# Optimization experiments

Measured on AMD Instinct MI355X. Metric: run time of the kernel, lower is better.

Reference implementation:

```python
import jax, jax.numpy as jnp
import numpy as np

NFFT = 512
SHIFT = 160
EPS = 1e-07
LOG10 = float(np.log(10.0))


def setup_inputs() -> dict:
    key = jax.random.key(0)
    x = jax.random.normal(key, (32, 1, 96512), dtype=jnp.float32)
    n = np.arange(NFFT)
    ang = 2.0 * np.pi * np.outer(n, n) / NFFT  # [k, n]
    W_real = np.cos(ang).astype(np.float32)
    W_imag = (-np.sin(ang)).astype(np.float32)
    return {"x": x, "W_real": jnp.asarray(W_real), "W_imag": jnp.asarray(W_imag)}


def reference(x, W_real, W_imag):
    # x: [B, C, T]; W_real/W_imag: [nfft, nfft] DFT basis (kernel k over taps n)
    B, C, T = x.shape
    n_frames = (T - NFFT) // SHIFT + 1
    # strided frame extraction == Conv1d(stride=SHIFT, kernel=NFFT) unfolding
    idx = jnp.arange(n_frames)[:, None] * SHIFT + jnp.arange(NFFT)[None, :]  # [F, N]
    frames = x[:, :, idx]  # [B, C, F, N]
    real = jnp.einsum('bcfn,kn->bckf', frames, W_real)  # [B, C, nfft, F]
    imag = jnp.einsum('bcfn,kn->bckf', frames, W_imag)
    # mode == 'log': log10 of magnitude spectrogram (with epsilon inside sqrt)
    fft = jnp.log(jnp.sqrt(real * real + imag * imag + EPS)) / LOG10
    fft = fft[:, :, : NFFT // 2, :]  # keep lower half of spectrum
    # normalize_feature: zero-mean, unit-std over frequency axis (biased std)
    mean = jnp.mean(fft, axis=2, keepdims=True)
    std = jnp.std(fft, axis=2, keepdims=True)
    return (fft - mean) / (std + EPS)
```

## Files before the change

kernel.cpp:

```cpp
#include <hip/hip_runtime.h>
#include <stdint.h>

#define TLEN    96512
#define NBATCH  32
#define KOUT    256
#define SHIFT   160
#define NFRAMES 601
#define FT      61
#define NTILES  10
#define NKS     16
#define EPSF    1e-7f

typedef _Float16 f16;
typedef _Float16 half8 __attribute__((ext_vector_type(8)));
typedef float f32x16 __attribute__((ext_vector_type(16)));

#define SPAN      ((FT - 1) * SHIFT + 256)
#define UNITS     (SPAN / 8)
#define PLANE_B   (UNITS * 16)
#define LDS_RED   (4 * PLANE_B)
#define LDS_STAT  (LDS_RED + 2048)
#define LDS_TOTAL (LDS_STAT + 512)

__global__ __launch_bounds__(256) void split_w_kernel(
    const float* __restrict__ Wr, const float* __restrict__ Wi,
    f16* __restrict__ wsW)
{
    int id   = blockIdx.x * 256 + threadIdx.x;
    int lane = id & 63;
    int hl   = (id >> 6) & 1;
    int ri   = (id >> 7) & 1;
    int ks   = (id >> 8) & 15;
    int J    = (id >> 12) & 3;
    int par  = (id >> 14) & 1;
    int l31  = lane & 31, lhi = lane >> 5;
    int k = 2 * (J * 32 + l31) + par;
    int n = ks * 16 + lhi * 8;
    const float* src = (ri ? Wi : Wr) + k * 512 + n;
    f16 v[8];
    #pragma unroll
    for (int j = 0; j < 8; ++j) {
        float xv = src[j];
        f16 h = (f16)xv;
        v[j] = hl ? (f16)(xv - (float)h) : h;
    }
    int c = ((par * 4 + J) * 16 + ks) * 4 + ri * 2 + hl;
    *(half8*)(wsW + (size_t)c * 512 + (l31 * 2 + lhi) * 8) = *(half8*)v;
}

__device__ __forceinline__ void load_a(half8 (&a)[2][2][2],
    const f16* __restrict__ wsW, int par, int jb2, int laneoff, int ks)
{
    #pragma unroll
    for (int m = 0; m < 2; ++m)
      #pragma unroll
      for (int ri = 0; ri < 2; ++ri)
        #pragma unroll
        for (int hl = 0; hl < 2; ++hl) {
            int c = ((par * 4 + jb2 + m) * 16 + ks) * 4 + ri * 2 + hl;
            a[m][ri][hl] = *(const half8*)(wsW + (size_t)c * 512 + laneoff);
        }
}

__device__ __forceinline__ void load_b(half8 (&bb)[2][2],
    const char* smem, int par, int l31, int lhi, int ks)
{
    #pragma unroll
    for (int nf = 0; nf < 2; ++nf)
      #pragma unroll
      for (int hl = 0; hl < 2; ++hl) {
          int u  = (nf * 32 + l31) * 20 + ks * 2 + lhi;
          int up = u ^ ((u >> 3) & 7);
          bb[nf][hl] = *(const half8*)(smem + (par * 2 + hl) * PLANE_B + up * 16);
      }
}

__device__ __forceinline__ void do_mfma(f32x16 (&acc)[2][2][2],
    const half8 (&a)[2][2][2], const half8 (&bb)[2][2])
{
    #pragma unroll
    for (int m = 0; m < 2; ++m)
      #pragma unroll
      for (int nf = 0; nf < 2; ++nf)
        #pragma unroll
        for (int ri = 0; ri < 2; ++ri) {
            acc[m][nf][ri] = __builtin_amdgcn_mfma_f32_32x32x16_f16(
                a[m][ri][0], bb[nf][0], acc[m][nf][ri], 0, 0, 0);
            acc[m][nf][ri] = __builtin_amdgcn_mfma_f32_32x32x16_f16(
                a[m][ri][0], bb[nf][1], acc[m][nf][ri], 0, 0, 0);
            acc[m][nf][ri] = __builtin_amdgcn_mfma_f32_32x32x16_f16(
                a[m][ri][1], bb[nf][0], acc[m][nf][ri], 0, 0, 0);
        }
}

__global__ __launch_bounds__(256, 2) void dft_mfma_kernel(
    const f16* __restrict__ wsW, const float* __restrict__ x,
    float* __restrict__ out)
{
    __shared__ uint4 smem4[LDS_TOTAL / 16];
    char* smem = (char*)smem4;

    const int tid  = threadIdx.x;
    const int lane = tid & 63;
    const int w    = tid >> 6;
    const int l31  = lane & 31;
    const int lhi  = lane >> 5;
    const int b    = blockIdx.y;
    const int f0   = blockIdx.x * FT;
    const int par  = w & 1;
    const int jb2  = (w >> 1) * 2;
    const int laneoff = (l31 * 2 + lhi) * 8;

    half8 a0[2][2][2], a1[2][2][2], b0[2][2], b1[2][2];
    load_a(a0, wsW, par, jb2, laneoff, 0);

    {
        const float* __restrict__ xb = x + (size_t)b * TLEN;
        const int t0 = f0 * SHIFT;
        for (int u = tid; u < UNITS; u += 256) {
            int t = t0 + u * 8;
            float va[8], vb[8];
            if (t + 264 <= TLEN) {
                float4 p0 = *(const float4*)(xb + t);
                float4 p1 = *(const float4*)(xb + t + 4);
                float4 q0 = *(const float4*)(xb + t + 256);
                float4 q1 = *(const float4*)(xb + t + 260);
                va[0]=p0.x; va[1]=p0.y; va[2]=p0.z; va[3]=p0.w;
                va[4]=p1.x; va[5]=p1.y; va[6]=p1.z; va[7]=p1.w;
                vb[0]=q0.x; vb[1]=q0.y; vb[2]=q0.z; vb[3]=q0.w;
                vb[4]=q1.x; vb[5]=q1.y; vb[6]=q1.z; vb[7]=q1.w;
            } else {
                #pragma unroll
                for (int j = 0; j < 8; ++j) {
                    int ta = t + j, tb = t + 256 + j;
                    va[j] = (ta < TLEN) ? xb[ta] : 0.f;
                    vb[j] = (tb < TLEN) ? xb[tb] : 0.f;
                }
            }
            f16 eh[8], el[8], oh[8], ol[8];
            #pragma unroll
            for (int j = 0; j < 8; ++j) {
                float E = va[j] + vb[j], O = va[j] - vb[j];
                eh[j] = (f16)E; el[j] = (f16)(E - (float)eh[j]);
                oh[j] = (f16)O; ol[j] = (f16)(O - (float)oh[j]);
            }
            int up = u ^ ((u >> 3) & 7);
            *(half8*)(smem + 0 * PLANE_B + up * 16) = *(half8*)eh;
            *(half8*)(smem + 1 * PLANE_B + up * 16) = *(half8*)el;
            *(half8*)(smem + 2 * PLANE_B + up * 16) = *(half8*)oh;
            *(half8*)(smem + 3 * PLANE_B + up * 16) = *(half8*)ol;
        }
    }
    __syncthreads();

    f32x16 acc[2][2][2] = {};
    load_b(b0, smem, par, l31, lhi, 0);

    #pragma unroll
    for (int ks2 = 0; ks2 < NKS; ks2 += 2) {
        load_a(a1, wsW, par, jb2, laneoff, ks2 + 1);
        load_b(b1, smem, par, l31, lhi, ks2 + 1);
        do_mfma(acc, a0, b0);
        int k2 = (ks2 + 2 < NKS) ? ks2 + 2 : NKS - 1;
        load_a(a0, wsW, par, jb2, laneoff, k2);
        load_b(b0, smem, par, l31, lhi, k2);
        do_mfma(acc, a1, b1);
    }

    const float C = 0.15051499783199057f;
    float lg[2][2][16];
    float s1[2] = {0.f, 0.f}, s2[2] = {0.f, 0.f};
    #pragma unroll
    for (int m = 0; m < 2; ++m)
      #pragma unroll
      for (int nf = 0; nf < 2; ++nf)
        #pragma unroll
        for (int r = 0; r < 16; ++r) {
            float re = acc[m][nf][0][r], im = acc[m][nf][1][r];
            float lv = C * __log2f(re * re + im * im + EPSF);
            lg[m][nf][r] = lv;
            s1[nf] += lv;
            s2[nf] += lv * lv;
        }
    #pragma unroll
    for (int nf = 0; nf < 2; ++nf) {
        s1[nf] += __shfl_xor(s1[nf], 32);
        s2[nf] += __shfl_xor(s2[nf], 32);
    }
    float2* red = (float2*)(smem + LDS_RED);
    if (lane < 32) {
        red[(w * 2 + 0) * 32 + l31] = make_float2(s1[0], s2[0]);
        red[(w * 2 + 1) * 32 + l31] = make_float2(s1[1], s2[1]);
    }
    __syncthreads();
    float* stat = (float*)(smem + LDS_STAT);
    if (tid < 64) {
        float S1 = 0.f, S2 = 0.f;
        int nf = tid >> 5, c = tid & 31;
        #pragma unroll
        for (int ww = 0; ww < 4; ++ww) {
            float2 p = red[(ww * 2 + nf) * 32 + c];
            S1 += p.x; S2 += p.y;
        }
        float mean = S1 * (1.f / 256.f);
        float var  = fmaxf(S2 * (1.f / 256.f) - mean * mean, 0.f);
        stat[tid]      = mean;
        stat[64 + tid] = 1.f / (__builtin_sqrtf(var) + EPSF);
    }
    __syncthreads();

    #pragma unroll
    for (int nf = 0; nf < 2; ++nf) {
        int fl = nf * 32 + l31;
        int f  = f0 + fl;
        if (fl >= FT || f >= NFRAMES) continue;
        float mean = stat[fl], rstd = stat[64 + fl];
        #pragma unroll
        for (int m = 0; m < 2; ++m)
          #pragma unroll
          for (int r = 0; r < 16; ++r) {
              int k = 2 * ((w >> 1) * 64 + m * 32 + (r & 3) + 8 * (r >> 2) + 4 * lhi) + par;
              out[((size_t)b * KOUT + k) * NFRAMES + f] = (lg[m][nf][r] - mean) * rstd;
          }
    }
}

extern "C" void kernel_launch(void* const* d_in, const int* in_sizes, int n_in,
                              void* d_out, int out_size, void* d_ws, size_t ws_size,
                              hipStream_t stream) {
    const float* x  = (const float*)d_in[0];
    const float* Wr = (const float*)d_in[1];
    const float* Wi = (const float*)d_in[2];
    float* out = (float*)d_out;

    f16* wsW = (f16*)d_ws;

    split_w_kernel<<<128, 256, 0, stream>>>(Wr, Wi, wsW);

    dim3 grid(NTILES, NBATCH);
    dft_mfma_kernel<<<grid, 256, 0, stream>>>(wsW, x, out);
}
```

Baseline: 37.40 us.

## Retile DFT kernel to 76-frame tiles with 512-thread blocks filling one wave

Changes the frame tiling from 10 tiles of 61 frames to 8 tiles of 76 frames and doubles the block to 512 threads. Each wave now owns one 32-row k-block and three 32-frame N fragments instead of two k-blocks and two N fragments. The goal is a grid of 256 blocks, one per CU, so no CUs sit partly idle as they do with the uneven 320-block grid. In exchange, frames 76–95 of each tile are computed and thrown away, and their B operands read past the end of each LDS plane into the next one. The LDS footprint also grows to roughly 110 KB per block, and each wave reuses its A operands less.

```diff
diff --git a/kernel.cpp b/kernel.cpp
--- a/kernel.cpp
+++ b/kernel.cpp
@@ -6,8 +6,8 @@
 #define KOUT    256
 #define SHIFT   160
 #define NFRAMES 601
-#define FT      61
-#define NTILES  10
+#define FT      76
+#define NTILES  8
 #define NKS     16
 #define EPSF    1e-7f
 
@@ -15,12 +15,12 @@
 typedef _Float16 half8 __attribute__((ext_vector_type(8)));
 typedef float f32x16 __attribute__((ext_vector_type(16)));
 
-#define SPAN      ((FT - 1) * SHIFT + 256)
-#define UNITS     (SPAN / 8)
-#define PLANE_B   (UNITS * 16)
-#define LDS_RED   (4 * PLANE_B)
-#define LDS_STAT  (LDS_RED + 2048)
-#define LDS_TOTAL (LDS_STAT + 512)
+#define SPAN       ((FT - 1) * SHIFT + 256)
+#define UNITS      (SPAN / 8)
+#define PLANE_B    24576
+#define LDS_RED    104768
+#define LDS_STAT   (LDS_RED + 6144)
+#define LDS_TOTAL  (LDS_STAT + 768)
 
 __global__ __launch_bounds__(256) void split_w_kernel(
     const float* __restrict__ Wr, const float* __restrict__ Wi,
@@ -48,25 +48,23 @@
     *(half8*)(wsW + (size_t)c * 512 + (l31 * 2 + lhi) * 8) = *(half8*)v;
 }
 
-__device__ __forceinline__ void load_a(half8 (&a)[2][2][2],
-    const f16* __restrict__ wsW, int par, int jb2, int laneoff, int ks)
-{
-    #pragma unroll
-    for (int m = 0; m < 2; ++m)
-      #pragma unroll
-      for (int ri = 0; ri < 2; ++ri)
-        #pragma unroll
-        for (int hl = 0; hl < 2; ++hl) {
-            int c = ((par * 4 + jb2 + m) * 16 + ks) * 4 + ri * 2 + hl;
-            a[m][ri][hl] = *(const half8*)(wsW + (size_t)c * 512 + laneoff);
-        }
-}
-
-__device__ __forceinline__ void load_b(half8 (&bb)[2][2],
+__device__ __forceinline__ void load_a(half8 (&a)[2][2],
+    const f16* __restrict__ wsW, int par, int J, int laneoff, int ks)
+{
+    #pragma unroll
+    for (int ri = 0; ri < 2; ++ri)
+      #pragma unroll
+      for (int hl = 0; hl < 2; ++hl) {
+          int c = ((par * 4 + J) * 16 + ks) * 4 + ri * 2 + hl;
+          a[ri][hl] = *(const half8*)(wsW + (size_t)c * 512 + laneoff);
+      }
+}
+
+__device__ __forceinline__ void load_b(half8 (&bb)[3][2],
     const char* smem, int par, int l31, int lhi, int ks)
 {
     #pragma unroll
-    for (int nf = 0; nf < 2; ++nf)
+    for (int nf = 0; nf < 3; ++nf)
       #pragma unroll
       for (int hl = 0; hl < 2; ++hl) {
           int u  = (nf * 32 + l31) * 20 + ks * 2 + lhi;
@@ -75,25 +73,23 @@
       }
 }
 
-__device__ __forceinline__ void do_mfma(f32x16 (&acc)[2][2][2],
-    const half8 (&a)[2][2][2], const half8 (&bb)[2][2])
-{
-    #pragma unroll
-    for (int m = 0; m < 2; ++m)
-      #pragma unroll
-      for (int nf = 0; nf < 2; ++nf)
-        #pragma unroll
-        for (int ri = 0; ri < 2; ++ri) {
-            acc[m][nf][ri] = __builtin_amdgcn_mfma_f32_32x32x16_f16(
-                a[m][ri][0], bb[nf][0], acc[m][nf][ri], 0, 0, 0);
-            acc[m][nf][ri] = __builtin_amdgcn_mfma_f32_32x32x16_f16(
-                a[m][ri][0], bb[nf][1], acc[m][nf][ri], 0, 0, 0);
-            acc[m][nf][ri] = __builtin_amdgcn_mfma_f32_32x32x16_f16(
-                a[m][ri][1], bb[nf][0], acc[m][nf][ri], 0, 0, 0);
-        }
-}
-
-__global__ __launch_bounds__(256, 2) void dft_mfma_kernel(
+__device__ __forceinline__ void do_mfma(f32x16 (&acc)[3][2],
+    const half8 (&a)[2][2], const half8 (&bb)[3][2])
+{
+    #pragma unroll
+    for (int nf = 0; nf < 3; ++nf)
+      #pragma unroll
+      for (int ri = 0; ri < 2; ++ri) {
+          acc[nf][ri] = __builtin_amdgcn_mfma_f32_32x32x16_f16(
+              a[ri][0], bb[nf][0], acc[nf][ri], 0, 0, 0);
+          acc[nf][ri] = __builtin_amdgcn_mfma_f32_32x32x16_f16(
+              a[ri][0], bb[nf][1], acc[nf][ri], 0, 0, 0);
+          acc[nf][ri] = __builtin_amdgcn_mfma_f32_32x32x16_f16(
+              a[ri][1], bb[nf][0], acc[nf][ri], 0, 0, 0);
+      }
+}
+
+__global__ __launch_bounds__(512, 2) void dft_mfma_kernel(
     const f16* __restrict__ wsW, const float* __restrict__ x,
     float* __restrict__ out)
 {
@@ -108,16 +104,16 @@
     const int b    = blockIdx.y;
     const int f0   = blockIdx.x * FT;
     const int par  = w & 1;
-    const int jb2  = (w >> 1) * 2;
+    const int J    = w >> 1;
     const int laneoff = (l31 * 2 + lhi) * 8;
 
-    half8 a0[2][2][2], a1[2][2][2], b0[2][2], b1[2][2];
-    load_a(a0, wsW, par, jb2, laneoff, 0);
+    half8 a0[2][2], a1[2][2], b0[3][2], b1[3][2];
+    load_a(a0, wsW, par, J, laneoff, 0);
 
     {
         const float* __restrict__ xb = x + (size_t)b * TLEN;
         const int t0 = f0 * SHIFT;
-        for (int u = tid; u < UNITS; u += 256) {
+        for (int u = tid; u < UNITS; u += 512) {
             int t = t0 + u * 8;
             float va[8], vb[8];
             if (t + 264 <= TLEN) {
@@ -153,75 +149,72 @@
     }
     __syncthreads();
 
-    f32x16 acc[2][2][2] = {};
+    f32x16 acc[3][2] = {};
     load_b(b0, smem, par, l31, lhi, 0);
 
     #pragma unroll
     for (int ks2 = 0; ks2 < NKS; ks2 += 2) {
-        load_a(a1, wsW, par, jb2, laneoff, ks2 + 1);
+        load_a(a1, wsW, par, J, laneoff, ks2 + 1);
         load_b(b1, smem, par, l31, lhi, ks2 + 1);
         do_mfma(acc, a0, b0);
         int k2 = (ks2 + 2 < NKS) ? ks2 + 2 : NKS - 1;
-        load_a(a0, wsW, par, jb2, laneoff, k2);
+        load_a(a0, wsW, par, J, laneoff, k2);
         load_b(b0, smem, par, l31, lhi, k2);
         do_mfma(acc, a1, b1);
     }
 
     const float C = 0.15051499783199057f;
-    float lg[2][2][16];
-    float s1[2] = {0.f, 0.f}, s2[2] = {0.f, 0.f};
-    #pragma unroll
-    for (int m = 0; m < 2; ++m)
-      #pragma unroll
-      for (int nf = 0; nf < 2; ++nf)
-        #pragma unroll
-        for (int r = 0; r < 16; ++r) {
-            float re = acc[m][nf][0][r], im = acc[m][nf][1][r];
-            float lv = C * __log2f(re * re + im * im + EPSF);
-            lg[m][nf][r] = lv;
-            s1[nf] += lv;
-            s2[nf] += lv * lv;
-        }
-    #pragma unroll
-    for (int nf = 0; nf < 2; ++nf) {
+    float lg[3][16];
+    float s1[3] = {0.f, 0.f, 0.f}, s2[3] = {0.f, 0.f, 0.f};
+    #pragma unroll
+    for (int nf = 0; nf < 3; ++nf)
+      #pragma unroll
+      for (int r = 0; r < 16; ++r) {
+          float re = acc[nf][0][r], im = acc[nf][1][r];
+          float lv = C * __log2f(re * re + im * im + EPSF);
+          lg[nf][r] = lv;
+          s1[nf] += lv;
+          s2[nf] += lv * lv;
+      }
+    #pragma unroll
+    for (int nf = 0; nf < 3; ++nf) {
         s1[nf] += __shfl_xor(s1[nf], 32);
         s2[nf] += __shfl_xor(s2[nf], 32);
     }
     float2* red = (float2*)(smem + LDS_RED);
     if (lane < 32) {
-        red[(w * 2 + 0) * 32 + l31] = make_float2(s1[0], s2[0]);
-        red[(w * 2 + 1) * 32 + l31] = make_float2(s1[1], s2[1]);
+        #pragma unroll
+        for (int nf = 0; nf < 3; ++nf)
+            red[(w * 3 + nf) * 32 + l31] = make_float2(s1[nf], s2[nf]);
     }
     __syncthreads();
     float* stat = (float*)(smem + LDS_STAT);
-    if (tid < 64) {
+    if (tid < 96) {
         float S1 = 0.f, S2 = 0.f;
         int nf = tid >> 5, c = tid & 31;
         #pragma unroll
-        for (int ww = 0; ww < 4; ++ww) {
-            float2 p = red[(ww * 2 + nf) * 32 + c];
+        for (int ww = 0; ww < 8; ++ww) {
+            float2 p = red[(ww * 3 + nf) * 32 + c];
             S1 += p.x; S2 += p.y;
         }
         float mean = S1 * (1.f / 256.f);
         float var  = fmaxf(S2 * (1.f / 256.f) - mean * mean, 0.f);
         stat[tid]      = mean;
-        stat[64 + tid] = 1.f / (__builtin_sqrtf(var) + EPSF);
+        stat[96 + tid] = 1.f / (__builtin_sqrtf(var) + EPSF);
     }
     __syncthreads();
 
     #pragma unroll
-    for (int nf = 0; nf < 2; ++nf) {
+    for (int nf = 0; nf < 3; ++nf) {
         int fl = nf * 32 + l31;
         int f  = f0 + fl;
         if (fl >= FT || f >= NFRAMES) continue;
-        float mean = stat[fl], rstd = stat[64 + fl];
+        float mean = stat[fl], rstd = stat[96 + fl];
         #pragma unroll
-        for (int m = 0; m < 2; ++m)
-          #pragma unroll
-          for (int r = 0; r < 16; ++r) {
-              int k = 2 * ((w >> 1) * 64 + m * 32 + (r & 3) + 8 * (r >> 2) + 4 * lhi) + par;
-              out[((size_t)b * KOUT + k) * NFRAMES + f] = (lg[m][nf][r] - mean) * rstd;
-          }
+        for (int r = 0; r < 16; ++r) {
+            int k = 2 * (J * 32 + (r & 3) + 8 * (r >> 2) + 4 * lhi) + par;
+            out[((size_t)b * KOUT + k) * NFRAMES + f] = (lg[nf][r] - mean) * rstd;
+        }
     }
 }
 
@@ -238,5 +231,5 @@
     split_w_kernel<<<128, 256, 0, stream>>>(Wr, Wi, wsW);
 
     dim3 grid(NTILES, NBATCH);
-    dft_mfma_kernel<<<grid, 256, 0, stream>>>(wsW, x, out);
-}
+    dft_mfma_kernel<<<grid, 512, 0, stream>>>(wsW, x, out);
+}
```

Measured after the change: 33.92 us. 1.1x faster.
